# Optimization experiments

Hardware: AMD Instinct MI355X
Metric: run time of the kernel (lower is better)

## Reference

```python
import jax, jax.numpy as jnp
import numpy as np

N = 50000   # nodes
E = 600000  # edges (avg degree 12)
D = 128     # embedding_dim == hidden_features
L = 4       # depth


def setup_inputs() -> dict:
    key = jax.random.key(0)
    k0, k1, k2, k3 = jax.random.split(key, 4)
    scale = 1.0 / np.sqrt(D)
    node_embedding = jax.random.normal(k0, (N, D), jnp.float32)
    edge_index = jax.random.randint(k1, (2, E), 0, N, dtype=jnp.int32)
    Ws_rel = jax.random.normal(k2, (L, D, D), jnp.float32) * scale
    bs_rel = jnp.zeros((L, D), jnp.float32)
    Ws_root = jax.random.normal(k3, (L, D, D), jnp.float32) * scale
    return {
        'node_embedding': node_embedding,
        'edge_index': edge_index,
        'Ws_rel': Ws_rel,
        'bs_rel': bs_rel,
        'Ws_root': Ws_root,
    }


def reference(node_embedding, edge_index, Ws_rel, bs_rel, Ws_root):
    # PyG GraphConv (aggr='mean'), flow source_to_target:
    #   out_i = lin_rel(mean_{j in N(i)} x_j) + lin_root(x_i)
    # followed by ELU (dropout probs are 0 -> identity).
    n = node_embedding.shape[0]
    src, dst = edge_index[0], edge_index[1]
    ones = jnp.ones((edge_index.shape[1],), node_embedding.dtype)
    deg = jax.ops.segment_sum(ones, dst, num_segments=n)
    inv_deg = (1.0 / jnp.maximum(deg, 1.0))[:, None]  # [n, 1]
    X = node_embedding
    for l in range(Ws_rel.shape[0]):
        agg = jax.ops.segment_sum(X[src], dst, num_segments=n) * inv_deg  # [n, D]
        out = agg @ Ws_rel[l] + bs_rel[l] + X @ Ws_root[l]
        X = jax.nn.elu(out)
    return X
```

## Files before the change

kernel.cpp:

```cpp
#include <hip/hip_runtime.h>

#define D 128
#define LDR 264
#define SLOTS 64
#define EPB 2048

typedef short bf16x8 __attribute__((ext_vector_type(8)));
typedef float f32x4 __attribute__((ext_vector_type(4)));

__device__ __forceinline__ unsigned short f2bf(float f) {
  unsigned int u = __float_as_uint(f);
  unsigned int r = (u + 0x7fff + ((u >> 16) & 1)) >> 16;
  return (unsigned short)r;
}
__device__ __forceinline__ unsigned int pack2bf(float lo, float hi) {
  return (unsigned int)f2bf(lo) | ((unsigned int)f2bf(hi) << 16);
}

__global__ __launch_bounds__(256) void k_build(
    const int* __restrict__ src, const int* __restrict__ dst, int E, int N,
    int* __restrict__ cursor, unsigned short* __restrict__ csr64,
    const float* __restrict__ X0, unsigned short* __restrict__ Xb, int total4,
    const float* __restrict__ Wrel, const float* __restrict__ Wroot,
    unsigned short* __restrict__ Wp, int wtot,
    int fb, int cb) {
  int b = blockIdx.x;
  if (b < fb) {
    int p = b & 7;
    int chunk = b >> 3;
    int lo = (int)((long long)p * N / 8);
    int hi = (int)((long long)(p + 1) * N / 8);
    int base = chunk * EPB + threadIdx.x;
#pragma unroll
    for (int it = 0; it < EPB / 256; ++it, base += 256) {
      if (base < E) {
        int d = dst[base];
        if (d >= lo && d < hi) {
          int ps = atomicAdd(&cursor[d], 1);
          if (ps < SLOTS) csr64[d * SLOTS + ps] = (unsigned short)src[base];
        }
      }
    }
    return;
  }
  b -= fb;
  if (b < cb) {
    int i = b * 256 + threadIdx.x;
    if (i < total4) {
      float4 v = ((const float4*)X0)[i];
      ushort4 o;
      o.x = f2bf(v.x); o.y = f2bf(v.y); o.z = f2bf(v.z); o.w = f2bf(v.w);
      ((ushort4*)Xb)[i] = o;
    }
    return;
  }
  b -= cb;
  {
    int gid = b * 256 + threadIdx.x;
    if (gid >= wtot) return;
    int lane = gid & 63;
    int t = gid >> 6;
    int ctg = t & 7; t >>= 3;
    int ks = t & 7; t >>= 3;
    int l = t;
    const float* Wr = Wrel + (size_t)l * D * D;
    const float* Wo = Wroot + (size_t)l * D * D;
    int colc = ctg * 16 + (lane & 15);
    int krow0 = ks * 32 + (lane >> 4) * 8;
    unsigned short tmp[8];
#pragma unroll
    for (int j = 0; j < 8; ++j) {
      int kr = krow0 + j;
      float w = (kr < D) ? Wr[(size_t)kr * D + colc] : Wo[(size_t)(kr - D) * D + colc];
      tmp[j] = f2bf(w);
    }
    unsigned short* dstp = Wp + ((size_t)gid) * 8;
#pragma unroll
    for (int j = 0; j < 8; ++j) dstp[j] = tmp[j];
  }
}


#define ACC8(v) \
    acc[0] += __uint_as_float((v).x << 16); acc[1] += __uint_as_float((v).x & 0xffff0000u); \
    acc[2] += __uint_as_float((v).y << 16); acc[3] += __uint_as_float((v).y & 0xffff0000u); \
    acc[4] += __uint_as_float((v).z << 16); acc[5] += __uint_as_float((v).z & 0xffff0000u); \
    acc[6] += __uint_as_float((v).w << 16); acc[7] += __uint_as_float((v).w & 0xffff0000u);

__global__ __launch_bounds__(256, 4) void k_layer_fused(
    const unsigned short* __restrict__ Xin,
    const int* __restrict__ cursor, const unsigned short* __restrict__ csr64,
    const unsigned short* __restrict__ Wp_l, const float* __restrict__ bias,
    unsigned short* __restrict__ Xnext, float* __restrict__ out_f32,
    int last, int N) {
  __shared__ __align__(16) unsigned short sRow[64 * LDR];
  int tid = threadIdx.x;
  int r0 = blockIdx.x * 64;
  int wave = tid >> 6, lane = tid & 63;
  int grp = lane >> 4;
  int l16 = lane & 15;

  int deg[4];
  uint2 bkt[4];
  uint4 vroot[4];
#pragma unroll
  for (int s = 0; s < 4; ++s) {
    int node = r0 + wave * 16 + s * 4 + grp;
    bool val = node < N;
    deg[s] = val ? cursor[node] : 0;
    bkt[s] = val ? *(const uint2*)(csr64 + (size_t)node * SLOTS + l16 * 4)
                 : make_uint2(0u, 0u);
    vroot[s] = val ? *(const uint4*)(Xin + (size_t)node * D + l16 * 8)
                   : make_uint4(0u, 0u, 0u, 0u);
  }

#pragma unroll
  for (int s = 0; s < 4; ++s) {
    int r = wave * 16 + s * 4 + grp;
    *(uint4*)(&sRow[r * LDR + (16 + l16) * 8]) = vroot[s];

    float acc[8];
#pragma unroll
    for (int t = 0; t < 8; ++t) acc[t] = 0.f;

    int n = min(deg[s], SLOTS);
    for (int j = 0; j < n; j += 8) {
      int a = grp * 16 + (j >> 2);
      unsigned ua_x = (unsigned)__shfl((int)bkt[s].x, a);
      unsigned ua_y = (unsigned)__shfl((int)bkt[s].y, a);
      unsigned ub_x = (unsigned)__shfl((int)bkt[s].x, a + 1);
      unsigned ub_y = (unsigned)__shfl((int)bkt[s].y, a + 1);
      int e[8];
      e[0] = (int)(ua_x & 0xffffu); e[1] = (int)(ua_x >> 16);
      e[2] = (int)(ua_y & 0xffffu); e[3] = (int)(ua_y >> 16);
      e[4] = (int)(ub_x & 0xffffu); e[5] = (int)(ub_x >> 16);
      e[6] = (int)(ub_y & 0xffffu); e[7] = (int)(ub_y >> 16);
      uint4 vv[8];
#pragma unroll
      for (int t = 0; t < 8; ++t) {
        int idx = (j + t < n) ? e[t] : 0;
        vv[t] = *(const uint4*)(Xin + (size_t)idx * D + l16 * 8);
      }
#pragma unroll
      for (int t = 0; t < 8; ++t) {
        if (j + t < n) { ACC8(vv[t]) }
      }
    }

    float inv = 1.0f / fmaxf((float)deg[s], 1.0f);
    uint4 o;
    o.x = pack2bf(acc[0] * inv, acc[1] * inv);
    o.y = pack2bf(acc[2] * inv, acc[3] * inv);
    o.z = pack2bf(acc[4] * inv, acc[5] * inv);
    o.w = pack2bf(acc[6] * inv, acc[7] * inv);
    *(uint4*)(&sRow[r * LDR + l16 * 8]) = o;
  }
  __syncthreads();

  int m = l16, q = grp;
  int ct0 = wave * 2;

  f32x4 cacc[4][2];
#pragma unroll
  for (int g = 0; g < 4; ++g)
#pragma unroll
    for (int c = 0; c < 2; ++c) cacc[g][c] = (f32x4){0.f, 0.f, 0.f, 0.f};

  const unsigned short* arow = &sRow[m * LDR + q * 8];
#pragma unroll
  for (int ks = 0; ks < 8; ++ks) {
    bf16x8 b0 = *(const bf16x8*)(Wp_l + ((size_t)((ks * 8 + ct0 + 0) * 64 + lane)) * 8);
    bf16x8 b1 = *(const bf16x8*)(Wp_l + ((size_t)((ks * 8 + ct0 + 1) * 64 + lane)) * 8);
    bf16x8 a0 = *(const bf16x8*)(arow + ks * 32);
    bf16x8 a1 = *(const bf16x8*)(arow + 16 * LDR + ks * 32);
    bf16x8 a2 = *(const bf16x8*)(arow + 32 * LDR + ks * 32);
    bf16x8 a3 = *(const bf16x8*)(arow + 48 * LDR + ks * 32);
    cacc[0][0] = __builtin_amdgcn_mfma_f32_16x16x32_bf16(a0, b0, cacc[0][0], 0, 0, 0);
    cacc[0][1] = __builtin_amdgcn_mfma_f32_16x16x32_bf16(a0, b1, cacc[0][1], 0, 0, 0);
    cacc[1][0] = __builtin_amdgcn_mfma_f32_16x16x32_bf16(a1, b0, cacc[1][0], 0, 0, 0);
    cacc[1][1] = __builtin_amdgcn_mfma_f32_16x16x32_bf16(a1, b1, cacc[1][1], 0, 0, 0);
    cacc[2][0] = __builtin_amdgcn_mfma_f32_16x16x32_bf16(a2, b0, cacc[2][0], 0, 0, 0);
    cacc[2][1] = __builtin_amdgcn_mfma_f32_16x16x32_bf16(a2, b1, cacc[2][1], 0, 0, 0);
    cacc[3][0] = __builtin_amdgcn_mfma_f32_16x16x32_bf16(a3, b0, cacc[3][0], 0, 0, 0);
    cacc[3][1] = __builtin_amdgcn_mfma_f32_16x16x32_bf16(a3, b1, cacc[3][1], 0, 0, 0);
  }

#pragma unroll
  for (int g = 0; g < 4; ++g) {
#pragma unroll
    for (int c = 0; c < 2; ++c) {
      int col = (ct0 + c) * 16 + m;
      float bv = bias[col];
      int rbase = r0 + g * 16 + q * 4;
#pragma unroll
      for (int j = 0; j < 4; ++j) {
        int row = rbase + j;
        float v = cacc[g][c][j] + bv;
        float e = __expf(fminf(v, 0.f)) - 1.f;
        v = v > 0.f ? v : e;
        if (last) {
          if (row < N) out_f32[(size_t)row * D + col] = v;
        } else {
          unsigned int h = (unsigned int)f2bf(v);
          unsigned int nb = (unsigned int)__shfl_xor((int)h, 1);
          if (!(m & 1) && row < N)
            *(unsigned int*)(Xnext + (size_t)row * D + col) = h | (nb << 16);
        }
      }
    }
  }
}


extern "C" void kernel_launch(void* const* d_in, const int* in_sizes, int n_in,
                              void* d_out, int out_size, void* d_ws, size_t ws_size,
                              hipStream_t stream) {
  const float* X0    = (const float*)d_in[0];
  const int*   eidx  = (const int*)d_in[1];
  const float* Wrel  = (const float*)d_in[2];
  const float* brel  = (const float*)d_in[3];
  const float* Wroot = (const float*)d_in[4];
  float* out = (float*)d_out;

  const int N = in_sizes[0] / D;
  const int E = in_sizes[1] / 2;
  const int L = in_sizes[3] / D;
  const int* src = eidx;
  const int* dst = eidx + E;

  char* ws = (char*)d_ws;
  size_t off = 0;
  auto carve = [&](size_t bytes) -> void* {
    void* p = ws + off;
    off = (off + bytes + 255) & ~(size_t)255;
    return p;
  };
  unsigned short* Xb0  = (unsigned short*)carve((size_t)N * D * sizeof(unsigned short));
  unsigned short* Xb1  = (unsigned short*)carve((size_t)N * D * sizeof(unsigned short));
  unsigned short* Wp   = (unsigned short*)carve((size_t)L * 4096 * 8 * sizeof(unsigned short));
  int*            cursor = (int*)carve((size_t)N * sizeof(int));
  unsigned short* csr64  = (unsigned short*)carve((size_t)N * SLOTS * sizeof(unsigned short));
  (void)ws_size; (void)n_in; (void)out_size;

  hipMemsetAsync(cursor, 0, (size_t)N * sizeof(int), stream);

  const int chunks = (E + EPB - 1) / EPB;
  const int fb = chunks * 8;
  const int total4 = N * D / 4;
  const int cb = (total4 + 255) / 256;
  const int wtot = L * 4096;
  const int wb = (wtot + 255) / 256;
  k_build<<<fb + cb + wb, 256, 0, stream>>>(src, dst, E, N, cursor, csr64,
      X0, Xb0, total4, Wrel, Wroot, Wp, wtot, fb, cb);

  const int lb = (N + 63) / 64;

  const unsigned short* Xcur = Xb0;
  for (int l = 0; l < L; ++l) {
    int last = (l == L - 1) ? 1 : 0;
    unsigned short* Xnext = (Xcur == Xb0) ? Xb1 : Xb0;
    k_layer_fused<<<lb, 256, 0, stream>>>(Xcur, cursor, csr64,
        Wp + (size_t)l * 4096 * 8, brel + (size_t)l * D, Xnext, out, last, N);
    Xcur = Xnext;
  }
}
```

Before: 243.4 us.

## Halve rows per block, raise occupancy, add 4-wide gather tail

Each block of the fused layer kernel now handles 32 rows instead of 64. This halves shared memory use and the MFMA accumulator count, and the occupancy hint rises from 4 to 6 blocks per CU, so more gather loads can be in flight for latency hiding. The neighbour-gather loop gains a 4-edge path for short remainders so it no longer issues 8 loads when only a few are valid. Padded lanes now load the node's own row instead of row 0, which should hit cache. The cost is twice as many blocks, each reloading the weight fragments, so global weight traffic per row goes up.

```diff
diff --git a/kernel.cpp b/kernel.cpp
--- a/kernel.cpp
+++ b/kernel.cpp
@@ -2,6 +2,7 @@
 
 #define D 128
 #define LDR 264
+#define TR 32
 #define SLOTS 64
 #define EPB 2048
 
@@ -87,25 +88,25 @@
     acc[4] += __uint_as_float((v).z << 16); acc[5] += __uint_as_float((v).z & 0xffff0000u); \
     acc[6] += __uint_as_float((v).w << 16); acc[7] += __uint_as_float((v).w & 0xffff0000u);
 
-__global__ __launch_bounds__(256, 4) void k_layer_fused(
+__global__ __launch_bounds__(256, 6) void k_layer_fused(
     const unsigned short* __restrict__ Xin,
     const int* __restrict__ cursor, const unsigned short* __restrict__ csr64,
     const unsigned short* __restrict__ Wp_l, const float* __restrict__ bias,
     unsigned short* __restrict__ Xnext, float* __restrict__ out_f32,
     int last, int N) {
-  __shared__ __align__(16) unsigned short sRow[64 * LDR];
+  __shared__ __align__(16) unsigned short sRow[TR * LDR];
   int tid = threadIdx.x;
-  int r0 = blockIdx.x * 64;
+  int r0 = blockIdx.x * TR;
   int wave = tid >> 6, lane = tid & 63;
   int grp = lane >> 4;
   int l16 = lane & 15;
 
-  int deg[4];
-  uint2 bkt[4];
-  uint4 vroot[4];
-#pragma unroll
-  for (int s = 0; s < 4; ++s) {
-    int node = r0 + wave * 16 + s * 4 + grp;
+  int deg[2];
+  uint2 bkt[2];
+  uint4 vroot[2];
+#pragma unroll
+  for (int s = 0; s < 2; ++s) {
+    int node = r0 + wave * 8 + s * 4 + grp;
     bool val = node < N;
     deg[s] = val ? cursor[node] : 0;
     bkt[s] = val ? *(const uint2*)(csr64 + (size_t)node * SLOTS + l16 * 4)
@@ -115,8 +116,10 @@
   }
 
 #pragma unroll
-  for (int s = 0; s < 4; ++s) {
-    int r = wave * 16 + s * 4 + grp;
+  for (int s = 0; s < 2; ++s) {
+    int curnode = r0 + wave * 8 + s * 4 + grp;
+    int safe = (curnode < N) ? curnode : 0;
+    int r = wave * 8 + s * 4 + grp;
     *(uint4*)(&sRow[r * LDR + (16 + l16) * 8]) = vroot[s];
 
     float acc[8];
@@ -124,26 +127,44 @@
     for (int t = 0; t < 8; ++t) acc[t] = 0.f;
 
     int n = min(deg[s], SLOTS);
-    for (int j = 0; j < n; j += 8) {
+    int j = 0;
+    for (; j < n; j += 8) {
+      int rem = n - j;
       int a = grp * 16 + (j >> 2);
       unsigned ua_x = (unsigned)__shfl((int)bkt[s].x, a);
       unsigned ua_y = (unsigned)__shfl((int)bkt[s].y, a);
-      unsigned ub_x = (unsigned)__shfl((int)bkt[s].x, a + 1);
-      unsigned ub_y = (unsigned)__shfl((int)bkt[s].y, a + 1);
-      int e[8];
-      e[0] = (int)(ua_x & 0xffffu); e[1] = (int)(ua_x >> 16);
-      e[2] = (int)(ua_y & 0xffffu); e[3] = (int)(ua_y >> 16);
-      e[4] = (int)(ub_x & 0xffffu); e[5] = (int)(ub_x >> 16);
-      e[6] = (int)(ub_y & 0xffffu); e[7] = (int)(ub_y >> 16);
-      uint4 vv[8];
-#pragma unroll
-      for (int t = 0; t < 8; ++t) {
-        int idx = (j + t < n) ? e[t] : 0;
-        vv[t] = *(const uint4*)(Xin + (size_t)idx * D + l16 * 8);
-      }
-#pragma unroll
-      for (int t = 0; t < 8; ++t) {
-        if (j + t < n) { ACC8(vv[t]) }
+      if (rem > 4) {
+        unsigned ub_x = (unsigned)__shfl((int)bkt[s].x, a + 1);
+        unsigned ub_y = (unsigned)__shfl((int)bkt[s].y, a + 1);
+        int e[8];
+        e[0] = (int)(ua_x & 0xffffu); e[1] = (int)(ua_x >> 16);
+        e[2] = (int)(ua_y & 0xffffu); e[3] = (int)(ua_y >> 16);
+        e[4] = (int)(ub_x & 0xffffu); e[5] = (int)(ub_x >> 16);
+        e[6] = (int)(ub_y & 0xffffu); e[7] = (int)(ub_y >> 16);
+        uint4 vv[8];
+#pragma unroll
+        for (int t = 0; t < 8; ++t) {
+          int idx = (j + t < n) ? e[t] : safe;
+          vv[t] = *(const uint4*)(Xin + (size_t)idx * D + l16 * 8);
+        }
+#pragma unroll
+        for (int t = 0; t < 8; ++t) {
+          if (j + t < n) { ACC8(vv[t]) }
+        }
+      } else {
+        int e[4];
+        e[0] = (int)(ua_x & 0xffffu); e[1] = (int)(ua_x >> 16);
+        e[2] = (int)(ua_y & 0xffffu); e[3] = (int)(ua_y >> 16);
+        uint4 vv[4];
+#pragma unroll
+        for (int t = 0; t < 4; ++t) {
+          int idx = (j + t < n) ? e[t] : safe;
+          vv[t] = *(const uint4*)(Xin + (size_t)idx * D + l16 * 8);
+        }
+#pragma unroll
+        for (int t = 0; t < 4; ++t) {
+          if (j + t < n) { ACC8(vv[t]) }
+        }
       }
     }
 
@@ -160,9 +181,9 @@
   int m = l16, q = grp;
   int ct0 = wave * 2;
 
-  f32x4 cacc[4][2];
-#pragma unroll
-  for (int g = 0; g < 4; ++g)
+  f32x4 cacc[2][2];
+#pragma unroll
+  for (int g = 0; g < 2; ++g)
 #pragma unroll
     for (int c = 0; c < 2; ++c) cacc[g][c] = (f32x4){0.f, 0.f, 0.f, 0.f};
 
@@ -173,20 +194,14 @@
     bf16x8 b1 = *(const bf16x8*)(Wp_l + ((size_t)((ks * 8 + ct0 + 1) * 64 + lane)) * 8);
     bf16x8 a0 = *(const bf16x8*)(arow + ks * 32);
     bf16x8 a1 = *(const bf16x8*)(arow + 16 * LDR + ks * 32);
-    bf16x8 a2 = *(const bf16x8*)(arow + 32 * LDR + ks * 32);
-    bf16x8 a3 = *(const bf16x8*)(arow + 48 * LDR + ks * 32);
     cacc[0][0] = __builtin_amdgcn_mfma_f32_16x16x32_bf16(a0, b0, cacc[0][0], 0, 0, 0);
     cacc[0][1] = __builtin_amdgcn_mfma_f32_16x16x32_bf16(a0, b1, cacc[0][1], 0, 0, 0);
     cacc[1][0] = __builtin_amdgcn_mfma_f32_16x16x32_bf16(a1, b0, cacc[1][0], 0, 0, 0);
     cacc[1][1] = __builtin_amdgcn_mfma_f32_16x16x32_bf16(a1, b1, cacc[1][1], 0, 0, 0);
-    cacc[2][0] = __builtin_amdgcn_mfma_f32_16x16x32_bf16(a2, b0, cacc[2][0], 0, 0, 0);
-    cacc[2][1] = __builtin_amdgcn_mfma_f32_16x16x32_bf16(a2, b1, cacc[2][1], 0, 0, 0);
-    cacc[3][0] = __builtin_amdgcn_mfma_f32_16x16x32_bf16(a3, b0, cacc[3][0], 0, 0, 0);
-    cacc[3][1] = __builtin_amdgcn_mfma_f32_16x16x32_bf16(a3, b1, cacc[3][1], 0, 0, 0);
-  }
-
-#pragma unroll
-  for (int g = 0; g < 4; ++g) {
+  }
+
+#pragma unroll
+  for (int g = 0; g < 2; ++g) {
 #pragma unroll
     for (int c = 0; c < 2; ++c) {
       int col = (ct0 + c) * 16 + m;
@@ -253,7 +268,7 @@
   k_build<<<fb + cb + wb, 256, 0, stream>>>(src, dst, E, N, cursor, csr64,
       X0, Xb0, total4, Wrel, Wroot, Wp, wtot, fb, cb);
 
-  const int lb = (N + 63) / 64;
+  const int lb = (N + TR - 1) / TR;
 
   const unsigned short* Xcur = Xb0;
   for (int l = 0; l < L; ++l) {
```

After: 236.9 us. 2.7% less time.
